# Kernel optimization log

Hardware: AMD Instinct MI355X
Metric: run time of the kernel (lower is better)

The kernel has to match this reference:

```python
import jax, jax.numpy as jnp
import numpy as np

B, S, D, H = 16, 512, 1024, 16
DH = D // H  # 64


def setup_inputs() -> dict:
    key = jax.random.key(0)
    kx, kq, kk, kv = jax.random.split(key, 4)
    stdv = 1.0 / np.sqrt(DH)  # reset_param uses 1/sqrt(t.size(1)) = 1/sqrt(head_dim)
    x = jax.random.normal(kx, (B, S, D), dtype=jnp.float32)
    Wq = jax.random.uniform(kq, (H, D, DH), dtype=jnp.float32, minval=-stdv, maxval=stdv)
    Wk = jax.random.uniform(kk, (H, D, DH), dtype=jnp.float32, minval=-stdv, maxval=stdv)
    Wv = jax.random.uniform(kv, (H, D, DH), dtype=jnp.float32, minval=-stdv, maxval=stdv)
    return {"x": x, "Wq": Wq, "Wk": Wk, "Wv": Wv}


def reference(x, Wq, Wk, Wv):
    # x: [B, S, D]; Wq/Wk/Wv: [H, D, DH] (stacked per-head params)
    q = jnp.einsum('bsd,hde->bhse', x, Wq)  # [B,H,S,DH]
    k = jnp.einsum('bsd,hde->bhse', x, Wk)
    v = jnp.einsum('bsd,hde->bhse', x, Wv)
    # NOTE: original scales by sqrt(input_dim), not sqrt(head_dim)
    scale = 1.0 / jnp.sqrt(jnp.float32(D))
    scores = jnp.einsum('bhse,bhte->bhst', q, k) * scale  # [B,H,S,S]
    attn = jax.nn.softmax(scores, axis=-1)
    out = jnp.einsum('bhst,bhte->bhse', attn, v)  # [B,H,S,DH]
    # concat heads along feature dim (head order matches torch cat over loop)
    return out.transpose(0, 2, 1, 3).reshape(x.shape[0], x.shape[1], D)
```

## Files before the change

### kernel.cpp

```cpp
#include <hip/hip_runtime.h>
#include <math.h>

constexpr int B = 16, S = 512, D = 1024, H = 16, DH = 64;
constexpr int BH = B * H;

typedef short bf16x8 __attribute__((ext_vector_type(8)));
typedef float f32x4  __attribute__((ext_vector_type(4)));

__device__ __forceinline__ unsigned short f2bf(float f) {
    unsigned u = __float_as_uint(f);
    u += 0x7fff + ((u >> 16) & 1);
    return (unsigned short)(u >> 16);
}

__global__ __launch_bounds__(256) void convert_x(
    const float* __restrict__ x, unsigned short* __restrict__ xb)
{
    int i = blockIdx.x * 256 + threadIdx.x;
    float4 v = ((const float4*)x)[i];
    ushort4 o;
    o.x = f2bf(v.x); o.y = f2bf(v.y); o.z = f2bf(v.z); o.w = f2bf(v.w);
    ((ushort4*)xb)[i] = o;
}

__global__ __launch_bounds__(256) void convert_w(
    const float* __restrict__ Wq, const float* __restrict__ Wk,
    const float* __restrict__ Wv, unsigned short* __restrict__ WbT)
{
    __shared__ float tile[64][65];
    const int d0 = blockIdx.x * 64;
    const int h = blockIdx.y, m = blockIdx.z;
    const float* W = ((m == 0) ? Wq : (m == 1) ? Wk : Wv) + (size_t)h * D * DH;
    const int t = threadIdx.x;
    {
        int e = t & 63, dr = t >> 6;
        #pragma unroll
        for (int i = 0; i < 16; ++i) {
            int d = dr * 16 + i;
            tile[d][e] = W[(size_t)(d0 + d) * DH + e];
        }
    }
    __syncthreads();
    {
        int d = t & 63, er = t >> 6;
        unsigned short* out = WbT + (size_t)(m * H + h) * DH * D;
        #pragma unroll
        for (int i = 0; i < 16; ++i) {
            int e = er * 16 + i;
            out[(size_t)e * D + d0 + d] = f2bf(tile[d][e]);
        }
    }
}

#define VMC8  asm volatile("s_waitcnt vmcnt(8)" ::: "memory")
#define VMC4  asm volatile("s_waitcnt vmcnt(4)" ::: "memory")
#define VMC0  asm volatile("s_waitcnt vmcnt(0)" ::: "memory")
#define LGKM0 asm volatile("s_waitcnt lgkmcnt(0)" ::: "memory")
#define BARR  __builtin_amdgcn_s_barrier()

__device__ __forceinline__ void stage_half(
    const unsigned short* __restrict__ src, int grow0, int k0,
    unsigned short* dst, int t)
{
    #pragma unroll
    for (int r = 0; r < 2; ++r) {
        int row = r * 64 + (t >> 3);
        int gg = (t & 7) ^ (row & 7);
        __builtin_amdgcn_global_load_lds(
            (const __attribute__((address_space(1))) void*)
                (src + (size_t)(grow0 + row) * 1024 + k0 + gg * 8),
            (__attribute__((address_space(3))) void*)(dst + r * 4096 + t * 8),
            16, 0, 0);
    }
}

template<int MODE>
__device__ __forceinline__ void kiter(
    const unsigned short* __restrict__ xb,
    const unsigned short* __restrict__ WbT,
    unsigned short* As0, unsigned short* Bs0,
    f32x4 (&acc)[8][4], int kb,
    int r0, int n0, int t, int wr, int wc, int lane15, int quad)
{
    #pragma unroll
    for (int half = 0; half < 2; ++half) {
        const unsigned short* Ab = As0 + half * 16384;
        const unsigned short* Bb = Bs0 + half * 16384;
        unsigned short* AsT = half ? As0 + 16384 : As0;
        unsigned short* BsT = half ? Bs0 : Bs0 + 16384;
        const int arow = wr * 128, brow = wc * 64;
        const int kB = kb + (1 + half) * 64;
        const int kA = kb + (2 + half) * 64;
        const bool doB = !(MODE == 0 && half == 0) && !(MODE == 2 && half == 1);
        const bool doA = (MODE != 2);

        bf16x8 a0[4][2], a1[4][2], b0[2][2], b1[2][2];

        #pragma unroll
        for (int mt = 0; mt < 4; ++mt)
            #pragma unroll
            for (int ks = 0; ks < 2; ++ks) {
                int rl = arow + mt * 16 + lane15, gk = ks * 4 + quad;
                a0[mt][ks] = *(const bf16x8*)(Ab + rl * 64 + (gk ^ (rl & 7)) * 8);
            }
        #pragma unroll
        for (int nt = 0; nt < 2; ++nt)
            #pragma unroll
            for (int ks = 0; ks < 2; ++ks) {
                int rl = brow + nt * 16 + lane15, gk = ks * 4 + quad;
                b0[nt][ks] = *(const bf16x8*)(Bb + rl * 64 + (gk ^ (rl & 7)) * 8);
            }
        if (doB) stage_half(WbT, n0, kB, BsT, t);
        BARR; LGKM0;
        __builtin_amdgcn_s_setprio(1);
        #pragma unroll
        for (int mt = 0; mt < 4; ++mt)
            #pragma unroll
            for (int nt = 0; nt < 2; ++nt) {
                acc[mt][nt] = __builtin_amdgcn_mfma_f32_16x16x32_bf16(
                    a0[mt][0], b0[nt][0], acc[mt][nt], 0, 0, 0);
                acc[mt][nt] = __builtin_amdgcn_mfma_f32_16x16x32_bf16(
                    a0[mt][1], b0[nt][1], acc[mt][nt], 0, 0, 0);
            }
        __builtin_amdgcn_s_setprio(0);
        BARR;

        #pragma unroll
        for (int mt = 0; mt < 4; ++mt)
            #pragma unroll
            for (int ks = 0; ks < 2; ++ks) {
                int rl = arow + 64 + mt * 16 + lane15, gk = ks * 4 + quad;
                a1[mt][ks] = *(const bf16x8*)(Ab + rl * 64 + (gk ^ (rl & 7)) * 8);
            }
        if (doB) stage_half(WbT, n0 + 128, kB, BsT + 8192, t);
        BARR; LGKM0;
        __builtin_amdgcn_s_setprio(1);
        #pragma unroll
        for (int mt = 0; mt < 4; ++mt)
            #pragma unroll
            for (int nt = 0; nt < 2; ++nt) {
                acc[4 + mt][nt] = __builtin_amdgcn_mfma_f32_16x16x32_bf16(
                    a1[mt][0], b0[nt][0], acc[4 + mt][nt], 0, 0, 0);
                acc[4 + mt][nt] = __builtin_amdgcn_mfma_f32_16x16x32_bf16(
                    a1[mt][1], b0[nt][1], acc[4 + mt][nt], 0, 0, 0);
            }
        __builtin_amdgcn_s_setprio(0);
        BARR;

        #pragma unroll
        for (int j = 0; j < 2; ++j)
            #pragma unroll
            for (int ks = 0; ks < 2; ++ks) {
                int rl = brow + 32 + j * 16 + lane15, gk = ks * 4 + quad;
                b1[j][ks] = *(const bf16x8*)(Bb + rl * 64 + (gk ^ (rl & 7)) * 8);
            }
        if (doA) stage_half(xb, r0, kA, AsT, t);
        BARR; LGKM0;
        __builtin_amdgcn_s_setprio(1);
        #pragma unroll
        for (int mt = 0; mt < 4; ++mt)
            #pragma unroll
            for (int j = 0; j < 2; ++j) {
                acc[4 + mt][2 + j] = __builtin_amdgcn_mfma_f32_16x16x32_bf16(
                    a1[mt][0], b1[j][0], acc[4 + mt][2 + j], 0, 0, 0);
                acc[4 + mt][2 + j] = __builtin_amdgcn_mfma_f32_16x16x32_bf16(
                    a1[mt][1], b1[j][1], acc[4 + mt][2 + j], 0, 0, 0);
            }
        __builtin_amdgcn_s_setprio(0);
        BARR;

        if (doA) stage_half(xb, r0 + 128, kA, AsT + 8192, t);
        BARR; LGKM0;
        __builtin_amdgcn_s_setprio(1);
        #pragma unroll
        for (int mt = 0; mt < 4; ++mt)
            #pragma unroll
            for (int j = 0; j < 2; ++j) {
                acc[mt][2 + j] = __builtin_amdgcn_mfma_f32_16x16x32_bf16(
                    a0[mt][0], b1[j][0], acc[mt][2 + j], 0, 0, 0);
                acc[mt][2 + j] = __builtin_amdgcn_mfma_f32_16x16x32_bf16(
                    a0[mt][1], b1[j][1], acc[mt][2 + j], 0, 0, 0);
            }
        __builtin_amdgcn_s_setprio(0);
        if (half == 0) { if (MODE == 2) { VMC0; } else { VMC4; } }
        else           { if (MODE != 2) { VMC4; } }
        BARR;
    }
}

__global__ __launch_bounds__(512, 2) void qkv_gemm(
    const unsigned short* __restrict__ xb,
    const unsigned short* __restrict__ WbT,
    unsigned short* __restrict__ qkvb)
{
    __shared__ unsigned short As[2 * 16384];
    __shared__ unsigned short Bs[2 * 16384];

    const int t = threadIdx.x;
    const int w = t >> 6;
    const int wr = w >> 2, wc = w & 3;
    const int L = t & 63;
    const int lane15 = L & 15;
    const int quad = L >> 4;

    const int r0 = blockIdx.x * 256;
    const int n0 = blockIdx.y * 256;

    f32x4 acc[8][4] = {};

    stage_half(xb,  r0,       0,  As,                t);
    stage_half(xb,  r0 + 128, 0,  As + 8192,         t);
    stage_half(WbT, n0,       0,  Bs,                t);
    stage_half(WbT, n0 + 128, 0,  Bs + 8192,         t);
    stage_half(xb,  r0,       64, As + 16384,        t);
    stage_half(xb,  r0 + 128, 64, As + 16384 + 8192, t);
    stage_half(WbT, n0,       64, Bs + 16384,        t);
    stage_half(WbT, n0 + 128, 64, Bs + 16384 + 8192, t);
    VMC8;
    BARR;

    kiter<0>(xb, WbT, As, Bs, acc, 0, r0, n0, t, wr, wc, lane15, quad);
    #pragma unroll 1
    for (int it = 1; it < 7; ++it)
        kiter<1>(xb, WbT, As, Bs, acc, it * 128, r0, n0, t, wr, wc, lane15, quad);
    kiter<2>(xb, WbT, As, Bs, acc, 896, r0, n0, t, wr, wc, lane15, quad);

    const int m  = n0 >> 10;
    const int h  = ((n0 >> 6) + wc) & 15;
    const int bb_ = r0 >> 9;
    const int s0 = (r0 & 511) + wr * 128;

    if (m == 2) {
        unsigned short* outv = qkvb + ((size_t)(2 * BH) + (bb_ * H + h)) * (size_t)(S * DH);
        #pragma unroll
        for (int mt = 0; mt < 8; ++mt) {
            int srow = s0 + mt * 16 + quad * 4;
            #pragma unroll
            for (int nt = 0; nt < 4; ++nt) {
                int e = nt * 16 + lane15;
                ushort4 pk;
                pk.x = f2bf(acc[mt][nt][0]);
                pk.y = f2bf(acc[mt][nt][1]);
                pk.z = f2bf(acc[mt][nt][2]);
                pk.w = f2bf(acc[mt][nt][3]);
                *(ushort4*)(outv + (size_t)e * S + srow) = pk;
            }
        }
    } else {
        const float sc = (m == 0) ? 0.04508422002778011f : 1.0f;
        unsigned short* out = qkvb + ((size_t)m * BH + (bb_ * H + h)) * (size_t)(S * DH);
        #pragma unroll
        for (int mt = 0; mt < 8; ++mt) {
            #pragma unroll
            for (int nt = 0; nt < 4; ++nt) {
                int e = nt * 16 + lane15;
                #pragma unroll
                for (int r = 0; r < 4; ++r) {
                    int srow = s0 + mt * 16 + quad * 4 + r;
                    out[(size_t)srow * DH + e] = f2bf(acc[mt][nt][r] * sc);
                }
            }
        }
    }
}

__global__ __launch_bounds__(256) void attn_mfma(
    const unsigned short* __restrict__ qkvb, float* __restrict__ out)
{
    __shared__ unsigned short Qs[128 * 64];
    __shared__ unsigned short Ks[64 * 64];
    __shared__ unsigned short Vt[64 * 64];

    const int t = threadIdx.x;
    const int w = t >> 6;
    const int L = t & 63;
    const int lane15 = L & 15;
    const int quad = L >> 4;
    const int lrow8 = L >> 3;
    const int lg = L & 7;
    const int qr0 = blockIdx.x * 128;
    const int bh = blockIdx.y;
    const int b = bh >> 4, h = bh & 15;

    const unsigned short* qb = qkvb + (size_t)bh * S * DH;
    const unsigned short* kb = qkvb + (size_t)(BH + bh) * S * DH;
    const unsigned short* vt = qkvb + (size_t)(2 * BH + bh) * S * DH;

    #pragma unroll
    for (int i = 0; i < 4; ++i) {
        int base = w * 32 + i * 8;
        int r = base + lrow8;
        int gg = lg ^ (r & 7);
        const unsigned short* gp = qb + (size_t)(qr0 + r) * DH + gg * 8;
        __builtin_amdgcn_global_load_lds(
            (const __attribute__((address_space(1))) void*)gp,
            (__attribute__((address_space(3))) void*)(Qs + base * 64),
            16, 0, 0);
    }

    f32x4 o[2][4] = {};
    float plsum[2] = {0.f, 0.f};
    bf16x8 qf[2][2];

    for (int kt = 0; kt < S; kt += 64) {
        #pragma unroll
        for (int i = 0; i < 2; ++i) {
            int base = (w * 2 + i) * 8;
            int r = base + lrow8;
            int gr = (r & 32) | ((r & 12) << 1) | ((r & 16) >> 2) | (r & 3);
            int gg = lg ^ (r & 7);
            const unsigned short* gpk = kb + (size_t)(kt + gr) * DH + gg * 8;
            __builtin_amdgcn_global_load_lds(
                (const __attribute__((address_space(1))) void*)gpk,
                (__attribute__((address_space(3))) void*)(Ks + base * 64),
                16, 0, 0);
            const unsigned short* gpv = vt + (size_t)r * S + kt + gg * 8;
            __builtin_amdgcn_global_load_lds(
                (const __attribute__((address_space(1))) void*)gpv,
                (__attribute__((address_space(3))) void*)(Vt + base * 64),
                16, 0, 0);
        }
        __syncthreads();

        if (kt == 0) {
            #pragma unroll
            for (int mt = 0; mt < 2; ++mt)
                #pragma unroll
                for (int ks = 0; ks < 2; ++ks) {
                    int ml = w * 32 + mt * 16 + lane15;
                    int gk = ks * 4 + quad;
                    qf[mt][ks] = *(const bf16x8*)(Qs + ml * 64 + ((gk ^ (lane15 & 7)) * 8));
                }
        }

        f32x4 st[2][4] = {};
        #pragma unroll
        for (int ks = 0; ks < 2; ++ks) {
            int gk = ks * 4 + quad;
            bf16x8 kf[4];
            #pragma unroll
            for (int ct = 0; ct < 4; ++ct) {
                int kr = ct * 16 + lane15;
                kf[ct] = *(const bf16x8*)(Ks + kr * 64 + ((gk ^ (lane15 & 7)) * 8));
            }
            #pragma unroll
            for (int mt = 0; mt < 2; ++mt)
                #pragma unroll
                for (int ct = 0; ct < 4; ++ct)
                    st[mt][ct] = __builtin_amdgcn_mfma_f32_16x16x32_bf16(
                        kf[ct], qf[mt][ks], st[mt][ct], 0, 0, 0);
        }

        bf16x8 pB[2][2];
        #pragma unroll
        for (int mt = 0; mt < 2; ++mt) {
            float rs = 0.f;
            #pragma unroll
            for (int ct = 0; ct < 4; ++ct) {
                float p0 = exp2f(st[mt][ct][0]);
                float p1 = exp2f(st[mt][ct][1]);
                float p2 = exp2f(st[mt][ct][2]);
                float p3 = exp2f(st[mt][ct][3]);
                rs += (p0 + p1) + (p2 + p3);
                int hi = (ct & 1) * 4;
                pB[mt][ct >> 1][hi + 0] = (short)f2bf(p0);
                pB[mt][ct >> 1][hi + 1] = (short)f2bf(p1);
                pB[mt][ct >> 1][hi + 2] = (short)f2bf(p2);
                pB[mt][ct >> 1][hi + 3] = (short)f2bf(p3);
            }
            plsum[mt] += rs;
        }

        #pragma unroll
        for (int ks = 0; ks < 2; ++ks) {
            int gk = ks * 4 + quad;
            bf16x8 vf[4];
            #pragma unroll
            for (int nt = 0; nt < 4; ++nt) {
                int dh = nt * 16 + lane15;
                vf[nt] = *(const bf16x8*)(Vt + dh * 64 + ((gk ^ (lane15 & 7)) * 8));
            }
            #pragma unroll
            for (int mt = 0; mt < 2; ++mt)
                #pragma unroll
                for (int nt = 0; nt < 4; ++nt)
                    o[mt][nt] = __builtin_amdgcn_mfma_f32_16x16x32_bf16(
                        vf[nt], pB[mt][ks], o[mt][nt], 0, 0, 0);
        }
        __syncthreads();
    }

    #pragma unroll
    for (int mt = 0; mt < 2; ++mt) {
        float l = plsum[mt];
        l += __shfl_xor(l, 16, 64);
        l += __shfl_xor(l, 32, 64);
        float inv = 1.0f / l;
        int srow = qr0 + w * 32 + mt * 16 + lane15;
        float* op = out + (size_t)(b * S + srow) * D + h * DH;
        #pragma unroll
        for (int nt = 0; nt < 4; ++nt) {
            float4 v;
            v.x = o[mt][nt][0] * inv;
            v.y = o[mt][nt][1] * inv;
            v.z = o[mt][nt][2] * inv;
            v.w = o[mt][nt][3] * inv;
            *(float4*)(op + nt * 16 + quad * 4) = v;
        }
    }
}

extern "C" void kernel_launch(void* const* d_in, const int* in_sizes, int n_in,
                              void* d_out, int out_size, void* d_ws, size_t ws_size,
                              hipStream_t stream) {
    const float* x  = (const float*)d_in[0];
    const float* Wq = (const float*)d_in[1];
    const float* Wk = (const float*)d_in[2];
    const float* Wv = (const float*)d_in[3];
    float* outp = (float*)d_out;

    unsigned short* qkvb = (unsigned short*)d_ws;
    unsigned short* xb   = (unsigned short*)((char*)d_ws + 50331648);
    unsigned short* WbT  = (unsigned short*)((char*)d_ws + 67108864);

    convert_x<<<dim3((B * S * D / 4) / 256), 256, 0, stream>>>(x, xb);
    convert_w<<<dim3(D / 64, H, 3), 256, 0, stream>>>(Wq, Wk, Wv, WbT);
    qkv_gemm<<<dim3(B * S / 256, 3 * H * DH / 256), 512, 0, stream>>>(xb, WbT, qkvb);
    attn_mfma<<<dim3(S / 128, BH), 256, 0, stream>>>(qkvb, outp);
}
```

Baseline: 214.7 us.

## Double-buffer K/V tiles in attention and prefetch next tile during compute

The attention kernel now keeps two LDS buffers for K and V. It issues the global-to-LDS loads for the next key tile right after reading the current tile into registers, so memory latency overlaps with the QK and PV MFMAs. The kernel also packs probabilities with v_cvt_pk_bf16_f32 in place of the manual rounding, raises wave priority around the MFMA blocks, and drops the min-blocks hint on qkv_gemm's launch bounds. The cost is more LDS per block and more registers held for the prefetched fragments, which could reduce occupancy.

```diff
diff --git a/kernel.cpp b/kernel.cpp
--- a/kernel.cpp
+++ b/kernel.cpp
@@ -12,6 +12,12 @@
     u += 0x7fff + ((u >> 16) & 1);
     return (unsigned short)(u >> 16);
 }
+
+#define VMC8  asm volatile("s_waitcnt vmcnt(8)" ::: "memory")
+#define VMC4  asm volatile("s_waitcnt vmcnt(4)" ::: "memory")
+#define VMC0  asm volatile("s_waitcnt vmcnt(0)" ::: "memory")
+#define LGKM0 asm volatile("s_waitcnt lgkmcnt(0)" ::: "memory")
+#define BARR  __builtin_amdgcn_s_barrier()
 
 __global__ __launch_bounds__(256) void convert_x(
     const float* __restrict__ x, unsigned short* __restrict__ xb)
@@ -51,12 +57,6 @@
         }
     }
 }
-
-#define VMC8  asm volatile("s_waitcnt vmcnt(8)" ::: "memory")
-#define VMC4  asm volatile("s_waitcnt vmcnt(4)" ::: "memory")
-#define VMC0  asm volatile("s_waitcnt vmcnt(0)" ::: "memory")
-#define LGKM0 asm volatile("s_waitcnt lgkmcnt(0)" ::: "memory")
-#define BARR  __builtin_amdgcn_s_barrier()
 
 __device__ __forceinline__ void stage_half(
     const unsigned short* __restrict__ src, int grow0, int k0,
@@ -188,7 +188,7 @@
     }
 }
 
-__global__ __launch_bounds__(512, 2) void qkv_gemm(
+__global__ __launch_bounds__(512) void qkv_gemm(
     const unsigned short* __restrict__ xb,
     const unsigned short* __restrict__ WbT,
     unsigned short* __restrict__ qkvb)
@@ -264,12 +264,35 @@
     }
 }
 
+__device__ __forceinline__ void stage_kv(
+    const unsigned short* __restrict__ kb, const unsigned short* __restrict__ vt,
+    int kt, unsigned short* Kd, unsigned short* Vd, int w, int lrow8, int lg)
+{
+    #pragma unroll
+    for (int i = 0; i < 2; ++i) {
+        int base = (w * 2 + i) * 8;
+        int r = base + lrow8;
+        int gr = (r & 32) | ((r & 12) << 1) | ((r & 16) >> 2) | (r & 3);
+        int gg = lg ^ (r & 7);
+        __builtin_amdgcn_global_load_lds(
+            (const __attribute__((address_space(1))) void*)
+                (kb + (size_t)(kt + gr) * DH + gg * 8),
+            (__attribute__((address_space(3))) void*)(Kd + base * 64),
+            16, 0, 0);
+        __builtin_amdgcn_global_load_lds(
+            (const __attribute__((address_space(1))) void*)
+                (vt + (size_t)r * S + kt + gg * 8),
+            (__attribute__((address_space(3))) void*)(Vd + base * 64),
+            16, 0, 0);
+    }
+}
+
 __global__ __launch_bounds__(256) void attn_mfma(
     const unsigned short* __restrict__ qkvb, float* __restrict__ out)
 {
     __shared__ unsigned short Qs[128 * 64];
-    __shared__ unsigned short Ks[64 * 64];
-    __shared__ unsigned short Vt[64 * 64];
+    __shared__ unsigned short Ks[2][64 * 64];
+    __shared__ unsigned short Vt[2][64 * 64];
 
     const int t = threadIdx.x;
     const int w = t >> 6;
@@ -297,64 +320,61 @@
             (__attribute__((address_space(3))) void*)(Qs + base * 64),
             16, 0, 0);
     }
+    stage_kv(kb, vt, 0, &Ks[0][0], &Vt[0][0], w, lrow8, lg);
+    VMC0;
+    BARR;
+
+    bf16x8 qf[2][2];
+    #pragma unroll
+    for (int mt = 0; mt < 2; ++mt)
+        #pragma unroll
+        for (int ks = 0; ks < 2; ++ks) {
+            int ml = w * 32 + mt * 16 + lane15;
+            int gk = ks * 4 + quad;
+            qf[mt][ks] = *(const bf16x8*)(Qs + ml * 64 + ((gk ^ (lane15 & 7)) * 8));
+        }
 
     f32x4 o[2][4] = {};
     float plsum[2] = {0.f, 0.f};
-    bf16x8 qf[2][2];
-
+
+    #pragma unroll 2
     for (int kt = 0; kt < S; kt += 64) {
-        #pragma unroll
-        for (int i = 0; i < 2; ++i) {
-            int base = (w * 2 + i) * 8;
-            int r = base + lrow8;
-            int gr = (r & 32) | ((r & 12) << 1) | ((r & 16) >> 2) | (r & 3);
-            int gg = lg ^ (r & 7);
-            const unsigned short* gpk = kb + (size_t)(kt + gr) * DH + gg * 8;
-            __builtin_amdgcn_global_load_lds(
-                (const __attribute__((address_space(1))) void*)gpk,
-                (__attribute__((address_space(3))) void*)(Ks + base * 64),
-                16, 0, 0);
-            const unsigned short* gpv = vt + (size_t)r * S + kt + gg * 8;
-            __builtin_amdgcn_global_load_lds(
-                (const __attribute__((address_space(1))) void*)gpv,
-                (__attribute__((address_space(3))) void*)(Vt + base * 64),
-                16, 0, 0);
-        }
-        __syncthreads();
-
-        if (kt == 0) {
-            #pragma unroll
-            for (int mt = 0; mt < 2; ++mt)
-                #pragma unroll
-                for (int ks = 0; ks < 2; ++ks) {
-                    int ml = w * 32 + mt * 16 + lane15;
-                    int gk = ks * 4 + quad;
-                    qf[mt][ks] = *(const bf16x8*)(Qs + ml * 64 + ((gk ^ (lane15 & 7)) * 8));
-                }
-        }
-
-        f32x4 st[2][4] = {};
+        const int cur = (kt >> 6) & 1;
+        const int nxt = cur ^ 1;
+
+        bf16x8 kf[2][4], vf[2][4];
         #pragma unroll
         for (int ks = 0; ks < 2; ++ks) {
             int gk = ks * 4 + quad;
-            bf16x8 kf[4];
             #pragma unroll
             for (int ct = 0; ct < 4; ++ct) {
                 int kr = ct * 16 + lane15;
-                kf[ct] = *(const bf16x8*)(Ks + kr * 64 + ((gk ^ (lane15 & 7)) * 8));
-            }
+                kf[ks][ct] = *(const bf16x8*)(&Ks[cur][0] + kr * 64 + ((gk ^ (lane15 & 7)) * 8));
+                vf[ks][ct] = *(const bf16x8*)(&Vt[cur][0] + kr * 64 + ((gk ^ (lane15 & 7)) * 8));
+            }
+        }
+        __builtin_amdgcn_sched_barrier(0);
+
+        if (kt + 64 < S)
+            stage_kv(kb, vt, kt + 64, &Ks[nxt][0], &Vt[nxt][0], w, lrow8, lg);
+
+        f32x4 st[2][4] = {};
+        __builtin_amdgcn_s_setprio(1);
+        #pragma unroll
+        for (int ks = 0; ks < 2; ++ks)
             #pragma unroll
             for (int mt = 0; mt < 2; ++mt)
                 #pragma unroll
                 for (int ct = 0; ct < 4; ++ct)
                     st[mt][ct] = __builtin_amdgcn_mfma_f32_16x16x32_bf16(
-                        kf[ct], qf[mt][ks], st[mt][ct], 0, 0, 0);
-        }
+                        kf[ks][ct], qf[mt][ks], st[mt][ct], 0, 0, 0);
+        __builtin_amdgcn_s_setprio(0);
 
         bf16x8 pB[2][2];
         #pragma unroll
         for (int mt = 0; mt < 2; ++mt) {
             float rs = 0.f;
+            union { unsigned u[4]; bf16x8 v; } pu[2];
             #pragma unroll
             for (int ct = 0; ct < 4; ++ct) {
                 float p0 = exp2f(st[mt][ct][0]);
@@ -362,32 +382,30 @@
                 float p2 = exp2f(st[mt][ct][2]);
                 float p3 = exp2f(st[mt][ct][3]);
                 rs += (p0 + p1) + (p2 + p3);
-                int hi = (ct & 1) * 4;
-                pB[mt][ct >> 1][hi + 0] = (short)f2bf(p0);
-                pB[mt][ct >> 1][hi + 1] = (short)f2bf(p1);
-                pB[mt][ct >> 1][hi + 2] = (short)f2bf(p2);
-                pB[mt][ct >> 1][hi + 3] = (short)f2bf(p3);
-            }
+                unsigned lo, hi;
+                asm("v_cvt_pk_bf16_f32 %0, %1, %2" : "=v"(lo) : "v"(p0), "v"(p1));
+                asm("v_cvt_pk_bf16_f32 %0, %1, %2" : "=v"(hi) : "v"(p2), "v"(p3));
+                pu[ct >> 1].u[(ct & 1) * 2 + 0] = lo;
+                pu[ct >> 1].u[(ct & 1) * 2 + 1] = hi;
+            }
+            pB[mt][0] = pu[0].v;
+            pB[mt][1] = pu[1].v;
             plsum[mt] += rs;
         }
 
-        #pragma unroll
-        for (int ks = 0; ks < 2; ++ks) {
-            int gk = ks * 4 + quad;
-            bf16x8 vf[4];
-            #pragma unroll
-            for (int nt = 0; nt < 4; ++nt) {
-                int dh = nt * 16 + lane15;
-                vf[nt] = *(const bf16x8*)(Vt + dh * 64 + ((gk ^ (lane15 & 7)) * 8));
-            }
+        __builtin_amdgcn_s_setprio(1);
+        #pragma unroll
+        for (int ks = 0; ks < 2; ++ks)
             #pragma unroll
             for (int mt = 0; mt < 2; ++mt)
                 #pragma unroll
                 for (int nt = 0; nt < 4; ++nt)
                     o[mt][nt] = __builtin_amdgcn_mfma_f32_16x16x32_bf16(
-                        vf[nt], pB[mt][ks], o[mt][nt], 0, 0, 0);
-        }
-        __syncthreads();
+                        vf[ks][nt], pB[mt][ks], o[mt][nt], 0, 0, 0);
+        __builtin_amdgcn_s_setprio(0);
+
+        VMC0;
+        BARR;
     }
 
     #pragma unroll
```

New measurement: 213.7 us. No clear change (-0.4%).
